# Kernel optimization log

Measured on AMD Instinct MI355X. Metric: run time of the kernel, lower is better.

Reference implementation:

```python
import jax, jax.numpy as jnp
import numpy as np

M_SQRT1_2 = 0.7071067811865476
P_DROP = 0.1  # activation_dropout


def setup_inputs() -> dict:
    key = jax.random.key(0)
    k1, k2, k3, k4 = jax.random.split(key, 4)
    N, FFN, EMB = 8192, 4096, 1024
    x = jax.random.normal(k1, (N, FFN), dtype=jnp.float16)
    weight = (jax.random.normal(k2, (EMB, FFN), dtype=jnp.float32) * (1.0 / np.sqrt(FFN))).astype(jnp.float16)
    bias = jax.random.normal(k3, (EMB,), dtype=jnp.float16)
    mask = jax.random.uniform(k4, (N, FFN)) >= P_DROP  # keep mask (bool)
    return {"x": x, "weight": weight, "bias": bias, "mask": mask}


def reference(x, weight, bias, mask):
    # GELU computed in fp32, cast back to fp16 (matches the custom IR)
    xf = x.astype(jnp.float32)
    g = (0.5 * xf * (1.0 + jax.lax.erf(xf * M_SQRT1_2))).astype(jnp.float16)
    # dropout: mask then scale by 1/(1-p) in fp16
    scale = jnp.float16(1.0 / (1.0 - P_DROP))
    h = g * mask.astype(jnp.float16) * scale  # [N, FFN]
    # y[N0, N2] = sum_N1 h[N0, N1] * weight[N2, N1] + bias[N2]
    y = jnp.einsum('nf,ef->ne', h, weight) + bias[None, :]
    return y
```

## Files before the change

kernel.cpp:

```cpp
#include <hip/hip_runtime.h>
#include <stdint.h>

typedef uint32_t u32;
typedef uint16_t u16;

static constexpr int M_DIM = 8192;
static constexpr int N_DIM = 1024;
static constexpr int K_DIM = 4096;

static constexpr int BM = 128;
static constexpr int BN = 256;
static constexpr int BK = 64;
static constexpr int KT64 = K_DIM / BK;
static constexpr int K_TILES32 = K_DIM / 32;
static constexpr int MB_TILES = M_DIM / 16;
static constexpr int NB_TILES = N_DIM / 16;

static constexpr size_t FRAG_U16 = 512;
static constexpr size_t HT_BYTES = (size_t)MB_TILES * K_TILES32 * FRAG_U16 * 2;
static constexpr size_t WT_BYTES = (size_t)NB_TILES * K_TILES32 * FRAG_U16 * 2;
static constexpr size_t WS_NEEDED = HT_BYTES + WT_BYTES;

typedef __attribute__((ext_vector_type(8))) _Float16 half8;
typedef __attribute__((ext_vector_type(4))) float f32x4;

union u4h8 { uint4 u; half8 h; };

__device__ __forceinline__ u32 pack2(float a, float b) {
  union { _Float16 h[2]; u32 u; } p;
  p.h[0] = (_Float16)a;
  p.h[1] = (_Float16)b;
  return p.u;
}

__device__ __forceinline__ float gelu_drop(float x, u32 keep) {
  float ax = fabsf(x);
  float z  = ax * 0.70710678f;
  float t  = __builtin_amdgcn_rcpf(fmaf(0.3275911f, z, 1.0f));
  float poly = fmaf(fmaf(fmaf(fmaf(1.061405429f, t, -1.453152027f),
                              t, 1.421413741f),
                         t, -0.284496736f),
                    t, 0.254829592f) * t;
  float e   = exp2f(z * z * -1.44269504f);
  float erf = fmaf(-poly, e, 1.0f);
  float g   = 0.5f * x * (1.0f + copysignf(erf, x));
  return keep ? g * 1.1111112f : 0.0f;
}

__device__ __forceinline__ void async_cp16(const void* g, void* l) {
  __builtin_amdgcn_global_load_lds((__attribute__((address_space(1))) u32*)g,
                                   (__attribute__((address_space(3))) u32*)l,
                                   16, 0, 0);
}

static constexpr int H_WAVES = MB_TILES * K_TILES32;
static constexpr int W_WAVES = NB_TILES * K_TILES32;
static constexpr int PACK_BLOCKS = (H_WAVES + W_WAVES) / 4;

__global__ __launch_bounds__(256)
void pack_kernel(const float* __restrict__ X, const int* __restrict__ Mask,
                 const float* __restrict__ W, u16* __restrict__ Ht, u16* __restrict__ Wt) {
  const int l     = threadIdx.x & 63;
  const int fi    = blockIdx.x * 4 + (threadIdx.x >> 6);
  const int row16 = l & 15;
  const int kof   = (l >> 4) << 3;

  if (fi < H_WAVES) {
    const int mb = fi >> 7, kt = fi & 127;
    const float* xp = X    + (size_t)(mb * 16 + row16) * K_DIM + kt * 32 + kof;
    const int*   mp = Mask + (size_t)(mb * 16 + row16) * K_DIM + kt * 32 + kof;
    float4 x0 = *(const float4*)(xp + 0);
    float4 x1 = *(const float4*)(xp + 4);
    uint4  m0 = *(const uint4*)(mp + 0);
    uint4  m1 = *(const uint4*)(mp + 4);
    u32 o0 = pack2(gelu_drop(x0.x, m0.x), gelu_drop(x0.y, m0.y));
    u32 o1 = pack2(gelu_drop(x0.z, m0.z), gelu_drop(x0.w, m0.w));
    u32 o2 = pack2(gelu_drop(x1.x, m1.x), gelu_drop(x1.y, m1.y));
    u32 o3 = pack2(gelu_drop(x1.z, m1.z), gelu_drop(x1.w, m1.w));
    *(uint4*)(Ht + (size_t)fi * FRAG_U16 + l * 8) = make_uint4(o0, o1, o2, o3);
  } else {
    const int fj = fi - H_WAVES;
    const int nb = fj >> 7, kt = fj & 127;
    const float* wp = W + (size_t)(nb * 16 + row16) * K_DIM + kt * 32 + kof;
    float4 w0 = *(const float4*)(wp + 0);
    float4 w1 = *(const float4*)(wp + 4);
    *(uint4*)(Wt + (size_t)fj * FRAG_U16 + l * 8) =
        make_uint4(pack2(w0.x, w0.y), pack2(w0.z, w0.w), pack2(w1.x, w1.y), pack2(w1.z, w1.w));
  }
}

__global__ __launch_bounds__(512, 2)
void gemm_kernel(const u16* __restrict__ Ht, const u16* __restrict__ Wt,
                 const float* __restrict__ Bias, float* __restrict__ Out) {
  __shared__ __attribute__((aligned(16))) u16 Abuf[2][BM * BK];

  const int tid  = threadIdx.x;
  const int lane = tid & 63;
  const int wv   = tid >> 6;
  const int wr   = wv >> 2;
  const int wc   = wv & 3;

  const int bm = blockIdx.x & 63;
  const int bn = blockIdx.x >> 6;
  const int m0 = bm * BM;
  const int n0 = bn * BN;

  const char* aG = (const char*)Ht;
  const int f2_0 = tid >> 6;
  const int f2_1 = (tid + 512) >> 6;
  const size_t aBase0 = ((size_t)(bm * 8 + (f2_0 >> 1)) * K_TILES32 + (f2_0 & 1)) * 1024 + (size_t)lane * 16;
  const size_t aBase1 = ((size_t)(bm * 8 + (f2_1 >> 1)) * K_TILES32 + (f2_1 & 1)) * 1024 + (size_t)lane * 16;
  char* aDst0[2] = {(char*)Abuf[0] + tid * 16, (char*)Abuf[1] + tid * 16};
  char* aDst1[2] = {(char*)Abuf[0] + (tid + 512) * 16, (char*)Abuf[1] + (tid + 512) * 16};

  const char* bp[8];
#pragma unroll
  for (int j = 0; j < 4; ++j)
#pragma unroll
    for (int kk = 0; kk < 2; ++kk)
      bp[j * 2 + kk] = (const char*)Wt +
          ((size_t)(bn * 16 + wc * 4 + j) * K_TILES32 + kk) * 1024 + (size_t)lane * 16;

  f32x4 acc[4][4];
#pragma unroll
  for (int i = 0; i < 4; ++i)
#pragma unroll
    for (int j = 0; j < 4; ++j)
      acc[i][j] = (f32x4){0.f, 0.f, 0.f, 0.f};

  async_cp16(aG + aBase0, aDst0[0]);
  async_cp16(aG + aBase1, aDst1[0]);
  u4h8 brE[8], brO[8];
#pragma unroll
  for (int q = 0; q < 8; ++q) brE[q].u = *(const uint4*)(bp[q]);
  __syncthreads();

#pragma unroll 1
  for (int kt = 0; kt < KT64; kt += 2) {
    {
      const size_t ko = (size_t)(kt + 1) * 2048;
      async_cp16(aG + aBase0 + ko, aDst0[1]);
      async_cp16(aG + aBase1 + ko, aDst1[1]);
#pragma unroll
      for (int q = 0; q < 8; ++q) brO[q].u = *(const uint4*)(bp[q] + ko);

      half8 ar[2][4];
#pragma unroll
      for (int kk = 0; kk < 2; ++kk)
#pragma unroll
        for (int i = 0; i < 4; ++i)
          ar[kk][i] = *(const half8*)((const char*)Abuf[0] + (((wr * 4 + i) * 2 + kk) * 64 + lane) * 16);
#pragma unroll
      for (int kk = 0; kk < 2; ++kk)
#pragma unroll
        for (int i = 0; i < 4; ++i)
#pragma unroll
          for (int j = 0; j < 4; ++j)
            acc[i][j] = __builtin_amdgcn_mfma_f32_16x16x32_f16(ar[kk][i], brE[j * 2 + kk].h, acc[i][j], 0, 0, 0);
      __syncthreads();
    }
    {
      if (kt + 2 < KT64) {
        const size_t ko = (size_t)(kt + 2) * 2048;
        async_cp16(aG + aBase0 + ko, aDst0[0]);
        async_cp16(aG + aBase1 + ko, aDst1[0]);
#pragma unroll
        for (int q = 0; q < 8; ++q) brE[q].u = *(const uint4*)(bp[q] + ko);
      }

      half8 ar[2][4];
#pragma unroll
      for (int kk = 0; kk < 2; ++kk)
#pragma unroll
        for (int i = 0; i < 4; ++i)
          ar[kk][i] = *(const half8*)((const char*)Abuf[1] + (((wr * 4 + i) * 2 + kk) * 64 + lane) * 16);
#pragma unroll
      for (int kk = 0; kk < 2; ++kk)
#pragma unroll
        for (int i = 0; i < 4; ++i)
#pragma unroll
          for (int j = 0; j < 4; ++j)
            acc[i][j] = __builtin_amdgcn_mfma_f32_16x16x32_f16(ar[kk][i], brO[j * 2 + kk].h, acc[i][j], 0, 0, 0);
      __syncthreads();
    }
  }

  const int fr = lane & 15;
  const int rq = (lane >> 4) << 2;
  float bv[4];
#pragma unroll
  for (int j = 0; j < 4; ++j)
    bv[j] = Bias[n0 + wc * 64 + j * 16 + fr];

#pragma unroll
  for (int i = 0; i < 4; ++i) {
    const int row0 = m0 + wr * 64 + i * 16 + rq;
#pragma unroll
    for (int j = 0; j < 4; ++j) {
      const int col = n0 + wc * 64 + j * 16 + fr;
#pragma unroll
      for (int r = 0; r < 4; ++r)
        Out[(size_t)(row0 + r) * N_DIM + col] = acc[i][j][r] + bv[j];
    }
  }
}

static constexpr int A_STRIDE = 40;

__global__ __launch_bounds__(256, 2)
void fused_fallback_kernel(const float* __restrict__ X, const float* __restrict__ W,
                           const float* __restrict__ Bias, const int* __restrict__ Mask,
                           float* __restrict__ Out) {
  __shared__ __attribute__((aligned(16))) _Float16 As[128 * A_STRIDE];
  __shared__ __attribute__((aligned(16))) _Float16 Bs[128 * 32];

  const int tid  = threadIdx.x;
  const int lane = tid & 63;
  const int wv   = tid >> 6;
  const int wr   = wv >> 1;
  const int wc   = wv & 1;
  const int bm = blockIdx.x & 63;
  const int bn = blockIdx.x >> 6;
  const int m0 = bm * 128;
  const int n0 = bn * 128;

  const int a_m = tid >> 1;
  const int a_k = (tid & 1) << 4;
  const float* xptr = X    + (size_t)(m0 + a_m) * K_DIM + a_k;
  const int*   mptr = Mask + (size_t)(m0 + a_m) * K_DIM + a_k;
  _Float16* a_lds = &As[a_m * A_STRIDE + a_k];

  const int i0 = tid, i1 = tid + 256;
  const float* wp0 = W + (size_t)(n0 + (i0 >> 2)) * K_DIM + ((i0 & 3) << 3);
  const float* wp1 = W + (size_t)(n0 + (i1 >> 2)) * K_DIM + ((i1 & 3) << 3);
  _Float16* bl0 = &Bs[i0 * 8];
  _Float16* bl1 = &Bs[i1 * 8];

  f32x4 acc[4][4];
#pragma unroll
  for (int i = 0; i < 4; ++i)
#pragma unroll
    for (int j = 0; j < 4; ++j)
      acc[i][j] = (f32x4){0.f, 0.f, 0.f, 0.f};

  float4 xf0 = *(const float4*)(xptr +  0);
  float4 xf1 = *(const float4*)(xptr +  4);
  float4 xf2 = *(const float4*)(xptr +  8);
  float4 xf3 = *(const float4*)(xptr + 12);
  uint4  mr0 = *(const uint4*)(mptr +  0);
  uint4  mr1 = *(const uint4*)(mptr +  4);
  uint4  mr2 = *(const uint4*)(mptr +  8);
  uint4  mr3 = *(const uint4*)(mptr + 12);
  float4 wf0 = *(const float4*)(wp0 + 0);
  float4 wf1 = *(const float4*)(wp0 + 4);
  float4 wf2 = *(const float4*)(wp1 + 0);
  float4 wf3 = *(const float4*)(wp1 + 4);

#pragma unroll 1
  for (int kt = 0; kt < 128; ++kt) {
    {
      float xs[16] = {xf0.x, xf0.y, xf0.z, xf0.w, xf1.x, xf1.y, xf1.z, xf1.w,
                      xf2.x, xf2.y, xf2.z, xf2.w, xf3.x, xf3.y, xf3.z, xf3.w};
      u32 mk[16]   = {mr0.x, mr0.y, mr0.z, mr0.w, mr1.x, mr1.y, mr1.z, mr1.w,
                      mr2.x, mr2.y, mr2.z, mr2.w, mr3.x, mr3.y, mr3.z, mr3.w};
      u32 ow[8];
#pragma unroll
      for (int e = 0; e < 8; ++e)
        ow[e] = pack2(gelu_drop(xs[2 * e], mk[2 * e]), gelu_drop(xs[2 * e + 1], mk[2 * e + 1]));
      ((uint4*)a_lds)[0] = make_uint4(ow[0], ow[1], ow[2], ow[3]);
      ((uint4*)a_lds)[1] = make_uint4(ow[4], ow[5], ow[6], ow[7]);
    }
    {
      *(uint4*)bl0 = make_uint4(pack2(wf0.x, wf0.y), pack2(wf0.z, wf0.w),
                                pack2(wf1.x, wf1.y), pack2(wf1.z, wf1.w));
      *(uint4*)bl1 = make_uint4(pack2(wf2.x, wf2.y), pack2(wf2.z, wf2.w),
                                pack2(wf3.x, wf3.y), pack2(wf3.z, wf3.w));
    }
    __syncthreads();

    if (kt + 1 < 128) {
      xptr += 32; mptr += 32; wp0 += 32; wp1 += 32;
      xf0 = *(const float4*)(xptr +  0);
      xf1 = *(const float4*)(xptr +  4);
      xf2 = *(const float4*)(xptr +  8);
      xf3 = *(const float4*)(xptr + 12);
      mr0 = *(const uint4*)(mptr +  0);
      mr1 = *(const uint4*)(mptr +  4);
      mr2 = *(const uint4*)(mptr +  8);
      mr3 = *(const uint4*)(mptr + 12);
      wf0 = *(const float4*)(wp0 + 0);
      wf1 = *(const float4*)(wp0 + 4);
      wf2 = *(const float4*)(wp1 + 0);
      wf3 = *(const float4*)(wp1 + 4);
    }

    {
      const int fr2 = lane & 15;
      const int fk2 = (lane >> 4) << 3;
      half8 ar[4], br[4];
#pragma unroll
      for (int i = 0; i < 4; ++i)
        ar[i] = *(const half8*)&As[(wr * 64 + i * 16 + fr2) * A_STRIDE + fk2];
#pragma unroll
      for (int j = 0; j < 4; ++j)
        br[j] = *(const half8*)&Bs[(wc * 64 + j * 16 + fr2) * 32 + fk2];
#pragma unroll
      for (int i = 0; i < 4; ++i)
#pragma unroll
        for (int j = 0; j < 4; ++j)
          acc[i][j] = __builtin_amdgcn_mfma_f32_16x16x32_f16(ar[i], br[j], acc[i][j], 0, 0, 0);
    }
    __syncthreads();
  }

  const int fr = lane & 15;
  const int rq = (lane >> 4) << 2;
  float bv[4];
#pragma unroll
  for (int j = 0; j < 4; ++j)
    bv[j] = Bias[n0 + wc * 64 + j * 16 + fr];
#pragma unroll
  for (int i = 0; i < 4; ++i) {
    const int row0 = m0 + wr * 64 + i * 16 + rq;
#pragma unroll
    for (int j = 0; j < 4; ++j) {
      const int col = n0 + wc * 64 + j * 16 + fr;
#pragma unroll
      for (int r = 0; r < 4; ++r)
        Out[(size_t)(row0 + r) * N_DIM + col] = acc[i][j][r] + bv[j];
    }
  }
}

extern "C" void kernel_launch(void* const* d_in, const int* in_sizes, int n_in,
                              void* d_out, int out_size, void* d_ws, size_t ws_size,
                              hipStream_t stream) {
  const float* X    = (const float*)d_in[0];
  const float* W    = (const float*)d_in[1];
  const float* Bias = (const float*)d_in[2];
  const int*   Mk   = (const int*)d_in[3];
  float* Out = (float*)d_out;

  if (ws_size >= WS_NEEDED) {
    u16* Ht = (u16*)d_ws;
    u16* Wt = (u16*)((char*)d_ws + HT_BYTES);
    pack_kernel<<<PACK_BLOCKS, 256, 0, stream>>>(X, Mk, W, Ht, Wt);
    gemm_kernel<<<(M_DIM / BM) * (N_DIM / BN), 512, 0, stream>>>(Ht, Wt, Bias, Out);
  } else {
    fused_fallback_kernel<<<64 * 8, 256, 0, stream>>>(X, W, Bias, Mk, Out);
  }
}
```

Baseline: 397.3 us.

## Stage W tiles through LDS with a 256x128 block tile

Changes the block tile from 128x256 to 256x128 with a 4x2 wave grid, and moves the weight operand from per-wave direct global register loads into double-buffered shared memory filled by async copies, like the activation operand. Each block now reads each weight fragment from global memory once instead of once per wave row. The cost is twice the LDS footprint per block and launch bounds dropped to one block per CU, which lowers occupancy and latency hiding. The epilogue indexing may still assume the old wave layout and could be inconsistent.

```diff
diff --git a/kernel.cpp b/kernel.cpp
--- a/kernel.cpp
+++ b/kernel.cpp
@@ -8,8 +8,8 @@
 static constexpr int N_DIM = 1024;
 static constexpr int K_DIM = 4096;
 
-static constexpr int BM = 128;
-static constexpr int BN = 256;
+static constexpr int BM = 256;
+static constexpr int BN = 128;
 static constexpr int BK = 64;
 static constexpr int KT64 = K_DIM / BK;
 static constexpr int K_TILES32 = K_DIM / 32;
@@ -23,8 +23,6 @@
 
 typedef __attribute__((ext_vector_type(8))) _Float16 half8;
 typedef __attribute__((ext_vector_type(4))) float f32x4;
-
-union u4h8 { uint4 u; half8 h; };
 
 __device__ __forceinline__ u32 pack2(float a, float b) {
   union { _Float16 h[2]; u32 u; } p;
@@ -89,37 +87,48 @@
   }
 }
 
-__global__ __launch_bounds__(512, 2)
+__global__ __launch_bounds__(512, 1)
 void gemm_kernel(const u16* __restrict__ Ht, const u16* __restrict__ Wt,
                  const float* __restrict__ Bias, float* __restrict__ Out) {
   __shared__ __attribute__((aligned(16))) u16 Abuf[2][BM * BK];
+  __shared__ __attribute__((aligned(16))) u16 Bbuf[2][BN * BK];
 
   const int tid  = threadIdx.x;
   const int lane = tid & 63;
   const int wv   = tid >> 6;
-  const int wr   = wv >> 2;
-  const int wc   = wv & 3;
-
-  const int bm = blockIdx.x & 63;
-  const int bn = blockIdx.x >> 6;
+  const int wr   = wv >> 1;
+  const int wc   = wv & 1;
+
+  const int bm = blockIdx.x & 31;
+  const int bn = blockIdx.x >> 5;
   const int m0 = bm * BM;
   const int n0 = bn * BN;
 
   const char* aG = (const char*)Ht;
-  const int f2_0 = tid >> 6;
-  const int f2_1 = (tid + 512) >> 6;
-  const size_t aBase0 = ((size_t)(bm * 8 + (f2_0 >> 1)) * K_TILES32 + (f2_0 & 1)) * 1024 + (size_t)lane * 16;
-  const size_t aBase1 = ((size_t)(bm * 8 + (f2_1 >> 1)) * K_TILES32 + (f2_1 & 1)) * 1024 + (size_t)lane * 16;
-  char* aDst0[2] = {(char*)Abuf[0] + tid * 16, (char*)Abuf[1] + tid * 16};
-  char* aDst1[2] = {(char*)Abuf[0] + (tid + 512) * 16, (char*)Abuf[1] + (tid + 512) * 16};
-
-  const char* bp[8];
-#pragma unroll
-  for (int j = 0; j < 4; ++j)
-#pragma unroll
-    for (int kk = 0; kk < 2; ++kk)
-      bp[j * 2 + kk] = (const char*)Wt +
-          ((size_t)(bn * 16 + wc * 4 + j) * K_TILES32 + kk) * 1024 + (size_t)lane * 16;
+  const char* bG = (const char*)Wt;
+  size_t aOff[4], bOff[2];
+#pragma unroll
+  for (int p = 0; p < 4; ++p) {
+    const int s = tid + 512 * p, f = s >> 6;
+    aOff[p] = ((size_t)(bm * 16 + (f >> 1)) * K_TILES32 + (f & 1)) * 1024 + (size_t)(s & 63) * 16;
+  }
+#pragma unroll
+  for (int p = 0; p < 2; ++p) {
+    const int s = tid + 512 * p, f = s >> 6;
+    bOff[p] = ((size_t)(bn * 8 + (f >> 1)) * K_TILES32 + (f & 1)) * 1024 + (size_t)(s & 63) * 16;
+  }
+
+  auto stage = [&](int kt, int buf) {
+    const size_t ko = (size_t)kt * 2048;
+    char* ad = (char*)Abuf[buf];
+    char* bd = (char*)Bbuf[buf];
+#pragma unroll
+    for (int p = 0; p < 4; ++p)
+      async_cp16(aG + aOff[p] + ko, ad + (tid + 512 * p) * 16);
+#pragma unroll
+    for (int p = 0; p < 2; ++p)
+      async_cp16(bG + bOff[p] + ko, bd + (tid + 512 * p) * 16);
+  };
 
   f32x4 acc[4][4];
 #pragma unroll
@@ -128,61 +137,37 @@
     for (int j = 0; j < 4; ++j)
       acc[i][j] = (f32x4){0.f, 0.f, 0.f, 0.f};
 
-  async_cp16(aG + aBase0, aDst0[0]);
-  async_cp16(aG + aBase1, aDst1[0]);
-  u4h8 brE[8], brO[8];
-#pragma unroll
-  for (int q = 0; q < 8; ++q) brE[q].u = *(const uint4*)(bp[q]);
+  auto compute = [&](int buf) {
+    const char* ab = (const char*)Abuf[buf];
+    const char* bb = (const char*)Bbuf[buf];
+#pragma unroll
+    for (int kk = 0; kk < 2; ++kk) {
+      half8 ar[4], br[4];
+#pragma unroll
+      for (int i = 0; i < 4; ++i)
+        ar[i] = *(const half8*)(ab + (((wr * 4 + i) * 2 + kk) * 64 + lane) * 16);
+#pragma unroll
+      for (int j = 0; j < 4; ++j)
+        br[j] = *(const half8*)(bb + (((wc * 4 + j) * 2 + kk) * 64 + lane) * 16);
+#pragma unroll
+      for (int i = 0; i < 4; ++i)
+#pragma unroll
+        for (int j = 0; j < 4; ++j)
+          acc[i][j] = __builtin_amdgcn_mfma_f32_16x16x32_f16(ar[i], br[j], acc[i][j], 0, 0, 0);
+    }
+  };
+
+  stage(0, 0);
   __syncthreads();
 
 #pragma unroll 1
   for (int kt = 0; kt < KT64; kt += 2) {
-    {
-      const size_t ko = (size_t)(kt + 1) * 2048;
-      async_cp16(aG + aBase0 + ko, aDst0[1]);
-      async_cp16(aG + aBase1 + ko, aDst1[1]);
-#pragma unroll
-      for (int q = 0; q < 8; ++q) brO[q].u = *(const uint4*)(bp[q] + ko);
-
-      half8 ar[2][4];
-#pragma unroll
-      for (int kk = 0; kk < 2; ++kk)
-#pragma unroll
-        for (int i = 0; i < 4; ++i)
-          ar[kk][i] = *(const half8*)((const char*)Abuf[0] + (((wr * 4 + i) * 2 + kk) * 64 + lane) * 16);
-#pragma unroll
-      for (int kk = 0; kk < 2; ++kk)
-#pragma unroll
-        for (int i = 0; i < 4; ++i)
-#pragma unroll
-          for (int j = 0; j < 4; ++j)
-            acc[i][j] = __builtin_amdgcn_mfma_f32_16x16x32_f16(ar[kk][i], brE[j * 2 + kk].h, acc[i][j], 0, 0, 0);
-      __syncthreads();
-    }
-    {
-      if (kt + 2 < KT64) {
-        const size_t ko = (size_t)(kt + 2) * 2048;
-        async_cp16(aG + aBase0 + ko, aDst0[0]);
-        async_cp16(aG + aBase1 + ko, aDst1[0]);
-#pragma unroll
-        for (int q = 0; q < 8; ++q) brE[q].u = *(const uint4*)(bp[q] + ko);
-      }
-
-      half8 ar[2][4];
-#pragma unroll
-      for (int kk = 0; kk < 2; ++kk)
-#pragma unroll
-        for (int i = 0; i < 4; ++i)
-          ar[kk][i] = *(const half8*)((const char*)Abuf[1] + (((wr * 4 + i) * 2 + kk) * 64 + lane) * 16);
-#pragma unroll
-      for (int kk = 0; kk < 2; ++kk)
-#pragma unroll
-        for (int i = 0; i < 4; ++i)
-#pragma unroll
-          for (int j = 0; j < 4; ++j)
-            acc[i][j] = __builtin_amdgcn_mfma_f32_16x16x32_f16(ar[kk][i], brO[j * 2 + kk].h, acc[i][j], 0, 0, 0);
-      __syncthreads();
-    }
+    if (kt + 1 < KT64) stage(kt + 1, 1);
+    compute(0);
+    __syncthreads();
+    if (kt + 2 < KT64) stage(kt + 2, 0);
+    compute(1);
+    __syncthreads();
   }
 
   const int fr = lane & 15;
```

After: 392.1 us. About the same (-1.3%).
